# Kernel tuning notes

Hardware: AMD Instinct MI355X
Metric: run time of the kernel (lower is better)

Reference implementation:

```python
import jax, jax.numpy as jnp
import numpy as np

B, L, DIM = 2, 2048, 2048
H, KV, HD = 32, 8, 64
N_REP = H // KV


def setup_inputs() -> dict:
    key = jax.random.key(0)
    ks = jax.random.split(key, 6)
    std = DIM ** -0.5
    std_o = (H * HD) ** -0.5 / np.sqrt(2 * 24)
    x = jax.random.normal(ks[0], (B, L, DIM), dtype=jnp.float32)
    # freqs_cis packs (cos, sin), each [L, head_dim//2]
    pos = jnp.arange(L, dtype=jnp.float32)[:, None]
    inv = 1.0 / (10000.0 ** (jnp.arange(0, HD, 2, dtype=jnp.float32) / HD))
    ang = pos * inv[None, :]
    freqs_cis = jnp.stack([jnp.cos(ang), jnp.sin(ang)], axis=0)
    wq = jax.random.normal(ks[1], (H * HD, DIM), dtype=jnp.float32) * std
    wk = jax.random.normal(ks[2], (KV * HD, DIM), dtype=jnp.float32) * std
    wv = jax.random.normal(ks[3], (KV * HD, DIM), dtype=jnp.float32) * std
    wo = jax.random.normal(ks[4], (DIM, H * HD), dtype=jnp.float32) * std_o
    return {"x": x, "freqs_cis": freqs_cis, "wq": wq, "wk": wk, "wv": wv, "wo": wo}


def _rope(t, cos, sin):
    # t: [B, L, h, HD]; interleaved (real, imag) pairs in last dim
    tr = t.reshape(*t.shape[:-1], HD // 2, 2)
    out_r = tr[..., 0] * cos - tr[..., 1] * sin
    out_i = tr[..., 0] * sin + tr[..., 1] * cos
    return jnp.stack([out_r, out_i], axis=-1).reshape(t.shape)


def reference(x, freqs_cis, wq, wk, wv, wo):
    Bb, Ll, _ = x.shape
    xq = (x @ wq.T).reshape(Bb, Ll, H, HD)
    xk = (x @ wk.T).reshape(Bb, Ll, KV, HD)
    xv = (x @ wv.T).reshape(Bb, Ll, KV, HD)
    cos = freqs_cis[0].reshape(1, Ll, 1, HD // 2)
    sin = freqs_cis[1].reshape(1, Ll, 1, HD // 2)
    xq = _rope(xq, cos, sin)
    xk = _rope(xk, cos, sin)
    # GQA: repeat_interleave kv heads to n_heads
    xk = jnp.repeat(xk, N_REP, axis=2)
    xv = jnp.repeat(xv, N_REP, axis=2)
    scale = 1.0 / jnp.sqrt(jnp.asarray(HD, x.dtype))
    scores = jnp.einsum('bihd,bjhd->bhij', xq, xk) * scale
    causal = jnp.tril(jnp.ones((Ll, Ll), dtype=bool))
    scores = jnp.where(causal[None, None], scores, jnp.finfo(scores.dtype).min)
    attn = jax.nn.softmax(scores, axis=-1)
    out = jnp.einsum('bhij,bjhd->bihd', attn, xv).reshape(Bb, Ll, H * HD)
    return out @ wo.T
```

## Files before the change

kernel.cpp:

```cpp
#include <hip/hip_runtime.h>
#include <stdint.h>

typedef __bf16 bf16;
typedef __attribute__((ext_vector_type(8))) __bf16 bf16x8;
typedef __attribute__((ext_vector_type(4))) __bf16 bf16x4;
typedef __attribute__((ext_vector_type(8))) short short8v;
typedef __attribute__((ext_vector_type(4))) short short4v;
typedef __attribute__((ext_vector_type(4))) float f32x4;

static constexpr int Bn = 2, Ln = 2048, DIMn = 2048, Hn = 32, KVn = 8, HDn = 64;
static constexpr int TS = 3072;

#if defined(__has_builtin)
#if __has_builtin(__builtin_amdgcn_exp2f)
#define EXP2(x) __builtin_amdgcn_exp2f(x)
#endif
#endif
#ifndef EXP2
#define EXP2(x) exp2f(x)
#endif

#define TO_LDS(p) ((__attribute__((address_space(3))) uint32_t*)(uintptr_t)(p))
#define TO_GLB(p) ((const __attribute__((address_space(1))) uint32_t*)(uintptr_t)(p))

__global__ void cast_all(const float* __restrict__ x, const float* __restrict__ wq,
                         const float* __restrict__ wk, const float* __restrict__ wv,
                         const float* __restrict__ wo, bf16* __restrict__ xb,
                         bf16* __restrict__ wqkvb, bf16* __restrict__ wob) {
    size_t i = (size_t)(blockIdx.x * blockDim.x + threadIdx.x) * 4;
    const float* src;
    bf16* dst;
    if (i < 8388608) {
        src = x + i; dst = xb + i;
    } else if (i < 8388608 + 6291456) {
        size_t j = i - 8388608;
        dst = wqkvb + j;
        if (j < 4194304)      src = wq + j;
        else if (j < 5242880) src = wk + (j - 4194304);
        else                  src = wv + (j - 5242880);
    } else {
        size_t j = i - 14680064;
        src = wo + j; dst = wob + j;
    }
    float4 v = *(const float4*)src;
    bf16 o[4] = {(bf16)v.x, (bf16)v.y, (bf16)v.z, (bf16)v.w};
    *(uint64_t*)dst = *(uint64_t*)o;
}

__global__ void rope_k(bf16* __restrict__ qkv, const float* __restrict__ fc) {
    int idx = blockIdx.x * blockDim.x + threadIdx.x;
    int i   = idx & 31;
    int kvh = (idx >> 5) & 7;
    int bl  = idx >> 8;
    int l   = bl & (Ln - 1);
    size_t base = (size_t)bl * TS + 2048 + kvh * 64 + 2 * i;
    float cr = fc[l * 32 + i];
    float sr = fc[65536 + l * 32 + i];
    float x0 = (float)qkv[base], x1 = (float)qkv[base + 1];
    qkv[base]     = (bf16)(x0 * cr - x1 * sr);
    qkv[base + 1] = (bf16)(x0 * sr + x1 * cr);
}

static __device__ __forceinline__ void barrier_f() {
    asm volatile("" ::: "memory");
    __builtin_amdgcn_s_barrier();
    asm volatile("" ::: "memory");
}

template <int N>
static __device__ __forceinline__ void waitcnt_vm() {
    if constexpr (N == 0) asm volatile("s_waitcnt vmcnt(0)" ::: "memory");
    else if constexpr (N == 6) asm volatile("s_waitcnt vmcnt(6)" ::: "memory");
    else if constexpr (N == 7) asm volatile("s_waitcnt vmcnt(7)" ::: "memory");
    else static_assert(N == 0 || N == 6 || N == 7, "add vmcnt literal");
}

template <int BM, int BN, bool OUT_BF16>
__global__ __launch_bounds__(512, 2) void gemm256(const bf16* __restrict__ A,
                                                  const bf16* __restrict__ Bm,
                                                  void* __restrict__ C,
                                                  int M, int N, int K) {
    (void)M;
    constexpr int MI = BM / 32;
    constexpr int NI = BN / 64;
    constexpr int AJ = BM / 64, BJ = BN / 64, LPT = AJ + BJ;
    __shared__ bf16 sA[2][BM * 64];
    __shared__ bf16 sB[2][BN * 64];
    const int t    = threadIdx.x;
    const int wave = t >> 6, lane = t & 63;
    const int q4 = lane >> 4, l16 = lane & 15;
    const int wm = wave >> 2, wn = wave & 3;
    const int r8l = lane >> 3;
    const int csw = ((lane & 7) ^ r8l) * 8;

    const size_t bm = (size_t)blockIdx.y * BM, bn = (size_t)blockIdx.x * BN;
    const bf16* pa = A  + (bm + (size_t)(wave * 8 + r8l)) * K + csw;
    const bf16* pb = Bm + (bn + (size_t)(wave * 8 + r8l)) * K + csw;
    const int NT = K >> 6;

#define STGA(buf, kt)                                                                          \
    _Pragma("unroll") for (int j = 0; j < AJ; ++j)                                             \
        __builtin_amdgcn_global_load_lds(TO_GLB(pa + (size_t)j * 64 * K + (size_t)(kt) * 64),  \
                                         TO_LDS(&sA[buf][(j * 64 + wave * 8) * 64]), 16, 0, 0)
#define STGB(buf, kt)                                                                          \
    _Pragma("unroll") for (int j = 0; j < BJ; ++j)                                             \
        __builtin_amdgcn_global_load_lds(TO_GLB(pb + (size_t)j * 64 * K + (size_t)(kt) * 64),  \
                                         TO_LDS(&sB[buf][(j * 64 + wave * 8) * 64]), 16, 0, 0)

    STGA(0, 0); STGB(0, 0);
    STGA(1, 1); STGB(1, 1);
    waitcnt_vm<LPT>();
    __builtin_amdgcn_s_barrier();
    asm volatile("" ::: "memory");

    f32x4 acc[MI][NI] = {};
    bf16x8 af[MI][2], bfr[NI][2];

    for (int k = 0; k < NT; ++k) {
        const int c = k & 1;
        const bf16* la = &sA[c][0];
        const bf16* lb = &sB[c][0];
        const int sw = (l16 & 7);

#pragma unroll
        for (int mi = 0; mi < MI / 2; ++mi)
#pragma unroll
            for (int kk = 0; kk < 2; ++kk)
                af[mi][kk] = *(const bf16x8*)(la + (wm * (BM / 2) + mi * 16 + l16) * 64 +
                                              ((kk * 4 + q4) ^ sw) * 8);
#pragma unroll
        for (int ni = 0; ni < NI; ++ni)
#pragma unroll
            for (int kk = 0; kk < 2; ++kk)
                bfr[ni][kk] = *(const bf16x8*)(lb + (wn * (BN / 4) + ni * 16 + l16) * 64 +
                                               ((kk * 4 + q4) ^ sw) * 8);
#pragma unroll
        for (int mi = MI / 2; mi < MI; ++mi)
#pragma unroll
            for (int kk = 0; kk < 2; ++kk)
                af[mi][kk] = *(const bf16x8*)(la + (wm * (BM / 2) + mi * 16 + l16) * 64 +
                                              ((kk * 4 + q4) ^ sw) * 8);

        __builtin_amdgcn_s_setprio(1);
#pragma unroll
        for (int mi = 0; mi < MI; ++mi)
#pragma unroll
            for (int ni = 0; ni < NI; ++ni)
#pragma unroll
                for (int kk = 0; kk < 2; ++kk)
                    acc[mi][ni] = __builtin_amdgcn_mfma_f32_16x16x32_bf16(
                        af[mi][kk], bfr[ni][kk], acc[mi][ni], 0, 0, 0);
        __builtin_amdgcn_s_setprio(0);

        barrier_f();

        if (k + 2 < NT) {
            STGA(c, k + 2);
            STGB(c, k + 2);
            waitcnt_vm<LPT>();
        } else if (k == NT - 2) {
            waitcnt_vm<0>();
        }
        barrier_f();
    }
#undef STGA
#undef STGB

#pragma unroll
    for (int mi = 0; mi < MI; ++mi)
#pragma unroll
        for (int ni = 0; ni < NI; ++ni)
#pragma unroll
            for (int r = 0; r < 4; ++r) {
                size_t row = bm + wm * (BM / 2) + mi * 16 + q4 * 4 + r;
                size_t col = bn + wn * (BN / 4) + ni * 16 + l16;
                if (OUT_BF16)
                    ((bf16*)C)[row * (size_t)N + col] = (bf16)acc[mi][ni][r];
                else
                    ((float*)C)[row * (size_t)N + col] = acc[mi][ni][r];
            }
}

__device__ __forceinline__ int swz(int row, int colbyte) {
    return row * 128 + (colbyte ^ ((row & 7) << 4));
}

__global__ __launch_bounds__(256, 2) void attn_kernel(const bf16* __restrict__ QKV,
                                                      const float* __restrict__ fc,
                                                      bf16* __restrict__ O) {
    __shared__ bf16 sK[64 * 64];
    __shared__ bf16 sV[64 * 64];
    const int t    = threadIdx.x;
    const int wave = t >> 6, lane = t & 63;
    const int q4 = lane >> 4, l16 = lane & 15;
    const int hidx = wave & 1, qh = wave >> 1;
    const int L = blockIdx.x;
    const int pair = L & 15, hp = (L >> 4) & 1, kvh = (L >> 5) & 7, b = L >> 8;
    const int h = kvh * 4 + hp * 2 + hidx;
    constexpr float SC = 0.125f * 1.44269504088896340736f;

    const bf16* kb = QKV + (size_t)(b * Ln) * TS + 2048 + kvh * 64;
    const bf16* vb = kb + 512;
    const int krow = t >> 3;
    const int kc8  = (t & 7) * 8;
    const int kp2  = (t & 31) * 2;
    const int vh8  = (t >> 5) * 8;

    for (int half = 0; half < 2; ++half) {
        const int qtile = half == 0 ? 31 - pair : pair;

        bf16x8 qf[2][2];
#pragma unroll
        for (int g2 = 0; g2 < 2; ++g2) {
            int ql = qtile * 64 + (qh * 2 + g2) * 16 + l16;
            const bf16* qp = QKV + (size_t)(b * Ln + ql) * TS + h * 64;
#pragma unroll
            for (int hc = 0; hc < 2; ++hc) {
                bf16x8 raw = *(const bf16x8*)(qp + hc * 32 + q4 * 8);
                float4 c4 = *(const float4*)(fc + ql * 32 + hc * 16 + q4 * 4);
                float4 s4 = *(const float4*)(fc + 65536 + ql * 32 + hc * 16 + q4 * 4);
                bf16x8 o;
#pragma unroll
                for (int m = 0; m < 4; ++m) {
                    float cr = ((const float*)&c4)[m], sr = ((const float*)&s4)[m];
                    float x0 = (float)raw[2 * m], x1 = (float)raw[2 * m + 1];
                    o[2 * m]     = (bf16)((x0 * cr - x1 * sr) * SC);
                    o[2 * m + 1] = (bf16)((x0 * sr + x1 * cr) * SC);
                }
                qf[g2][hc] = o;
            }
        }

        f32x4 o_acc[2][4] = {};
        float l_r[2] = {0.f, 0.f};

        bf16x8 kreg[2], vrA, vrB;
#pragma unroll
        for (int p = 0; p < 2; ++p)
            kreg[p] = *(const bf16x8*)(kb + (size_t)(p * 32 + krow) * TS + kc8);
        vrA = *(const bf16x8*)(vb + (size_t)kp2 * TS + vh8);
        vrB = *(const bf16x8*)(vb + (size_t)(kp2 + 1) * TS + vh8);

        for (int kt = 0; kt <= qtile; ++kt) {
#pragma unroll
            for (int p = 0; p < 2; ++p) {
                int row = p * 32 + krow;
                *(float4*)((char*)sK + swz(row, kc8 * 2)) = *(float4*)&kreg[p];
            }
            {
                short8v sa = __builtin_bit_cast(short8v, vrA);
                short8v sb = __builtin_bit_cast(short8v, vrB);
#pragma unroll
                for (int j = 0; j < 8; ++j) {
                    uint32_t d = (uint32_t)(uint16_t)sa[j] |
                                 ((uint32_t)(uint16_t)sb[j] << 16);
                    *(uint32_t*)((char*)sV + swz(vh8 + j, kp2 * 2)) = d;
                }
            }
            __syncthreads();

            if (kt < qtile) {
#pragma unroll
                for (int p = 0; p < 2; ++p)
                    kreg[p] = *(const bf16x8*)(kb + (size_t)((kt + 1) * 64 + p * 32 + krow) * TS + kc8);
                vrA = *(const bf16x8*)(vb + (size_t)((kt + 1) * 64 + kp2) * TS + vh8);
                vrB = *(const bf16x8*)(vb + (size_t)((kt + 1) * 64 + kp2 + 1) * TS + vh8);
            }

            bf16x8 kf[4][2];
#pragma unroll
            for (int c = 0; c < 4; ++c)
#pragma unroll
                for (int hc = 0; hc < 2; ++hc)
                    kf[c][hc] = *(const bf16x8*)((const char*)sK +
                                                 swz(c * 16 + l16, hc * 64 + q4 * 16));
            short4v vf[4][4];
#pragma unroll
            for (int nc = 0; nc < 4; ++nc)
#pragma unroll
                for (int c = 0; c < 4; ++c)
                    vf[nc][c] = *(const short4v*)((const char*)sV +
                                                  swz(nc * 16 + l16, c * 32 + q4 * 8));

            const bool diag = (kt == qtile);
#pragma unroll
            for (int g2 = 0; g2 < 2; ++g2) {
                f32x4 s[4];
                __builtin_amdgcn_s_setprio(1);
#pragma unroll
                for (int c = 0; c < 4; ++c) {
                    f32x4 a = {};
                    a = __builtin_amdgcn_mfma_f32_16x16x32_bf16(kf[c][0], qf[g2][0], a, 0, 0, 0);
                    a = __builtin_amdgcn_mfma_f32_16x16x32_bf16(kf[c][1], qf[g2][1], a, 0, 0, 0);
                    s[c] = a;
                }
                __builtin_amdgcn_s_setprio(0);
                int qrow = qtile * 64 + (qh * 2 + g2) * 16 + l16;
                float lsum = 0.f;
                short4v pb4[4];
                if (diag) {
#pragma unroll
                    for (int c = 0; c < 4; ++c) {
                        float pc[4];
#pragma unroll
                        for (int r = 0; r < 4; ++r) {
                            float p = EXP2(s[c][r] - 12.f);
                            if (kt * 64 + c * 16 + q4 * 4 + r > qrow) p = 0.f;
                            pc[r] = p;
                            bf16 ph = (bf16)p;
                            pb4[c][r] = *(const short*)&ph;
                        }
                        lsum += (pc[0] + pc[1]) + (pc[2] + pc[3]);
                    }
                } else {
#pragma unroll
                    for (int c = 0; c < 4; ++c) {
                        float pc[4];
#pragma unroll
                        for (int r = 0; r < 4; ++r) {
                            float p = EXP2(s[c][r] - 12.f);
                            pc[r] = p;
                            bf16 ph = (bf16)p;
                            pb4[c][r] = *(const short*)&ph;
                        }
                        lsum += (pc[0] + pc[1]) + (pc[2] + pc[3]);
                    }
                }
                l_r[g2] += lsum;
                __builtin_amdgcn_s_setprio(1);
#pragma unroll
                for (int nc = 0; nc < 4; ++nc)
#pragma unroll
                    for (int c = 0; c < 4; ++c)
                        o_acc[g2][nc] = __builtin_amdgcn_mfma_f32_16x16x16bf16_1k(
                            vf[nc][c], pb4[c], o_acc[g2][nc], 0, 0, 0);
                __builtin_amdgcn_s_setprio(0);
            }
            __syncthreads();
        }

#pragma unroll
        for (int g2 = 0; g2 < 2; ++g2) {
            float l = l_r[g2];
            l += __shfl_xor(l, 16, 64);
            l += __shfl_xor(l, 32, 64);
            float inv = 1.f / l;
            int qrow = qtile * 64 + (qh * 2 + g2) * 16 + l16;
            bf16* op = O + (size_t)(b * Ln + qrow) * (Hn * HDn) + h * 64;
#pragma unroll
            for (int nc = 0; nc < 4; ++nc) {
                bf16x4 o;
#pragma unroll
                for (int r = 0; r < 4; ++r) o[r] = (bf16)(o_acc[g2][nc][r] * inv);
                *(bf16x4*)(op + nc * 16 + q4 * 4) = o;
            }
        }
    }
}

extern "C" void kernel_launch(void* const* d_in, const int* in_sizes, int n_in,
                              void* d_out, int out_size, void* d_ws, size_t ws_size,
                              hipStream_t stream) {
    const float* x  = (const float*)d_in[0];
    const float* fc = (const float*)d_in[1];
    const float* wq = (const float*)d_in[2];
    const float* wk = (const float*)d_in[3];
    const float* wv = (const float*)d_in[4];
    const float* wo = (const float*)d_in[5];
    float* out = (float*)d_out;

    const size_t T = (size_t)Bn * Ln;
    char* p = (char*)d_ws;
    bf16* xb    = (bf16*)p; p += T * DIMn * 2;
    bf16* wqkvb = (bf16*)p; p += (size_t)TS * DIMn * 2;
    bf16* wob   = (bf16*)p; p += (size_t)DIMn * Hn * HDn * 2;
    bf16* qkv   = (bf16*)p; p += T * TS * 2;
    bf16* ao    = (bf16*)p; p += T * Hn * HDn * 2;

    cast_all<<<dim3(18432), dim3(256), 0, stream>>>(x, wq, wk, wv, wo, xb, wqkvb, wob);

    gemm256<256, 192, true><<<dim3(TS / 192, 4096 / 256), dim3(512), 0, stream>>>(
        xb, wqkvb, qkv, 4096, TS, 2048);

    rope_k<<<dim3(4096), dim3(256), 0, stream>>>(qkv, fc);

    attn_kernel<<<dim3(512), dim3(256), 0, stream>>>(qkv, fc, ao);

    gemm256<128, 256, false><<<dim3(2048 / 256, 4096 / 128), dim3(512), 0, stream>>>(
        ao, wob, out, 4096, 2048, 2048);
}
```

Before: 273.1 us.

## Replace large-tile GEMM with 128x128 tile, BK=32 kernel for both projections

Replaces the templated 512-thread GEMM (256x192 / 128x256 tiles, K-step 64) with a fixed 256-thread 128x128 tile kernel using K-step 32, a new LDS swizzle, and launch bounds allowing three blocks per CU. Both the QKV projection and output projection now launch more, smaller blocks, which improves wave count and occupancy on the 256-CU device. In exchange, each block reuses less data per tile and the loop runs twice as many barrier-separated iterations with less MFMA work per sync.

New measurement: 288.8 us. 5.7% more time.

```diff
diff --git a/kernel.cpp b/kernel.cpp
--- a/kernel.cpp
+++ b/kernel.cpp
@@ -70,110 +70,93 @@
 template <int N>
 static __device__ __forceinline__ void waitcnt_vm() {
     if constexpr (N == 0) asm volatile("s_waitcnt vmcnt(0)" ::: "memory");
-    else if constexpr (N == 6) asm volatile("s_waitcnt vmcnt(6)" ::: "memory");
-    else if constexpr (N == 7) asm volatile("s_waitcnt vmcnt(7)" ::: "memory");
-    else static_assert(N == 0 || N == 6 || N == 7, "add vmcnt literal");
-}
-
-template <int BM, int BN, bool OUT_BF16>
-__global__ __launch_bounds__(512, 2) void gemm256(const bf16* __restrict__ A,
+    else if constexpr (N == 4) asm volatile("s_waitcnt vmcnt(4)" ::: "memory");
+    else static_assert(N == 0 || N == 4, "add vmcnt literal");
+}
+
+template <bool OUT_BF16>
+__global__ __launch_bounds__(256, 3) void gemm128(const bf16* __restrict__ A,
                                                   const bf16* __restrict__ Bm,
                                                   void* __restrict__ C,
                                                   int M, int N, int K) {
     (void)M;
-    constexpr int MI = BM / 32;
-    constexpr int NI = BN / 64;
-    constexpr int AJ = BM / 64, BJ = BN / 64, LPT = AJ + BJ;
-    __shared__ bf16 sA[2][BM * 64];
-    __shared__ bf16 sB[2][BN * 64];
+    __shared__ bf16 sA[2][128 * 32];
+    __shared__ bf16 sB[2][128 * 32];
     const int t    = threadIdx.x;
     const int wave = t >> 6, lane = t & 63;
     const int q4 = lane >> 4, l16 = lane & 15;
-    const int wm = wave >> 2, wn = wave & 3;
-    const int r8l = lane >> 3;
-    const int csw = ((lane & 7) ^ r8l) * 8;
-
-    const size_t bm = (size_t)blockIdx.y * BM, bn = (size_t)blockIdx.x * BN;
-    const bf16* pa = A  + (bm + (size_t)(wave * 8 + r8l)) * K + csw;
-    const bf16* pb = Bm + (bn + (size_t)(wave * 8 + r8l)) * K + csw;
-    const int NT = K >> 6;
-
-#define STGA(buf, kt)                                                                          \
-    _Pragma("unroll") for (int j = 0; j < AJ; ++j)                                             \
-        __builtin_amdgcn_global_load_lds(TO_GLB(pa + (size_t)j * 64 * K + (size_t)(kt) * 64),  \
-                                         TO_LDS(&sA[buf][(j * 64 + wave * 8) * 64]), 16, 0, 0)
-#define STGB(buf, kt)                                                                          \
-    _Pragma("unroll") for (int j = 0; j < BJ; ++j)                                             \
-        __builtin_amdgcn_global_load_lds(TO_GLB(pb + (size_t)j * 64 * K + (size_t)(kt) * 64),  \
-                                         TO_LDS(&sB[buf][(j * 64 + wave * 8) * 64]), 16, 0, 0)
-
-    STGA(0, 0); STGB(0, 0);
-    STGA(1, 1); STGB(1, 1);
-    waitcnt_vm<LPT>();
+    const int wm = wave >> 1, wn = wave & 1;
+    const int srow = lane >> 2;
+    const int scol = ((lane & 3) ^ (srow & 3)) * 8;
+
+    const size_t bm = (size_t)blockIdx.y * 128, bn = (size_t)blockIdx.x * 128;
+    const bf16* pa = A  + (bm + (size_t)(wave * 16 + srow)) * K + scol;
+    const bf16* pb = Bm + (bn + (size_t)(wave * 16 + srow)) * K + scol;
+    const int NT = K >> 5;
+
+#define STG(buf, kt)                                                                           \
+    do {                                                                                       \
+        _Pragma("unroll") for (int j = 0; j < 2; ++j) {                                        \
+            __builtin_amdgcn_global_load_lds(                                                  \
+                TO_GLB(pa + (size_t)j * 64 * K + (size_t)(kt) * 32),                           \
+                TO_LDS(&sA[buf][(j * 64 + wave * 16) * 32]), 16, 0, 0);                        \
+            __builtin_amdgcn_global_load_lds(                                                  \
+                TO_GLB(pb + (size_t)j * 64 * K + (size_t)(kt) * 32),                           \
+                TO_LDS(&sB[buf][(j * 64 + wave * 16) * 32]), 16, 0, 0);                        \
+        }                                                                                      \
+    } while (0)
+
+    STG(0, 0);
+    STG(1, 1);
+    waitcnt_vm<4>();
     __builtin_amdgcn_s_barrier();
     asm volatile("" ::: "memory");
 
-    f32x4 acc[MI][NI] = {};
-    bf16x8 af[MI][2], bfr[NI][2];
+    f32x4 acc[4][4] = {};
+    bf16x8 af[4], bfr[4];
 
     for (int k = 0; k < NT; ++k) {
         const int c = k & 1;
-        const bf16* la = &sA[c][0];
-        const bf16* lb = &sB[c][0];
-        const int sw = (l16 & 7);
-
-#pragma unroll
-        for (int mi = 0; mi < MI / 2; ++mi)
-#pragma unroll
-            for (int kk = 0; kk < 2; ++kk)
-                af[mi][kk] = *(const bf16x8*)(la + (wm * (BM / 2) + mi * 16 + l16) * 64 +
-                                              ((kk * 4 + q4) ^ sw) * 8);
-#pragma unroll
-        for (int ni = 0; ni < NI; ++ni)
-#pragma unroll
-            for (int kk = 0; kk < 2; ++kk)
-                bfr[ni][kk] = *(const bf16x8*)(lb + (wn * (BN / 4) + ni * 16 + l16) * 64 +
-                                               ((kk * 4 + q4) ^ sw) * 8);
-#pragma unroll
-        for (int mi = MI / 2; mi < MI; ++mi)
-#pragma unroll
-            for (int kk = 0; kk < 2; ++kk)
-                af[mi][kk] = *(const bf16x8*)(la + (wm * (BM / 2) + mi * 16 + l16) * 64 +
-                                              ((kk * 4 + q4) ^ sw) * 8);
+        const int sw = l16 & 3;
+
+#pragma unroll
+        for (int mi = 0; mi < 4; ++mi)
+            af[mi] = *(const bf16x8*)(&sA[c][(wm * 64 + mi * 16 + l16) * 32 +
+                                             ((q4 ^ sw) * 8)]);
+#pragma unroll
+        for (int ni = 0; ni < 4; ++ni)
+            bfr[ni] = *(const bf16x8*)(&sB[c][(wn * 64 + ni * 16 + l16) * 32 +
+                                              ((q4 ^ sw) * 8)]);
 
         __builtin_amdgcn_s_setprio(1);
 #pragma unroll
-        for (int mi = 0; mi < MI; ++mi)
-#pragma unroll
-            for (int ni = 0; ni < NI; ++ni)
-#pragma unroll
-                for (int kk = 0; kk < 2; ++kk)
-                    acc[mi][ni] = __builtin_amdgcn_mfma_f32_16x16x32_bf16(
-                        af[mi][kk], bfr[ni][kk], acc[mi][ni], 0, 0, 0);
+        for (int mi = 0; mi < 4; ++mi)
+#pragma unroll
+            for (int ni = 0; ni < 4; ++ni)
+                acc[mi][ni] = __builtin_amdgcn_mfma_f32_16x16x32_bf16(
+                    af[mi], bfr[ni], acc[mi][ni], 0, 0, 0);
         __builtin_amdgcn_s_setprio(0);
 
         barrier_f();
 
         if (k + 2 < NT) {
-            STGA(c, k + 2);
-            STGB(c, k + 2);
-            waitcnt_vm<LPT>();
+            STG(c, k + 2);
+            waitcnt_vm<4>();
         } else if (k == NT - 2) {
             waitcnt_vm<0>();
         }
         barrier_f();
     }
-#undef STGA
-#undef STGB
-
-#pragma unroll
-    for (int mi = 0; mi < MI; ++mi)
-#pragma unroll
-        for (int ni = 0; ni < NI; ++ni)
+#undef STG
+
+#pragma unroll
+    for (int mi = 0; mi < 4; ++mi)
+#pragma unroll
+        for (int ni = 0; ni < 4; ++ni)
 #pragma unroll
             for (int r = 0; r < 4; ++r) {
-                size_t row = bm + wm * (BM / 2) + mi * 16 + q4 * 4 + r;
-                size_t col = bn + wn * (BN / 4) + ni * 16 + l16;
+                size_t row = bm + wm * 64 + mi * 16 + q4 * 4 + r;
+                size_t col = bn + wn * 64 + ni * 16 + l16;
                 if (OUT_BF16)
                     ((bf16*)C)[row * (size_t)N + col] = (bf16)acc[mi][ni][r];
                 else
@@ -379,13 +362,13 @@
 
     cast_all<<<dim3(18432), dim3(256), 0, stream>>>(x, wq, wk, wv, wo, xb, wqkvb, wob);
 
-    gemm256<256, 192, true><<<dim3(TS / 192, 4096 / 256), dim3(512), 0, stream>>>(
+    gemm128<true><<<dim3(TS / 128, 4096 / 128), dim3(256), 0, stream>>>(
         xb, wqkvb, qkv, 4096, TS, 2048);
 
     rope_k<<<dim3(4096), dim3(256), 0, stream>>>(qkv, fc);
 
     attn_kernel<<<dim3(512), dim3(256), 0, stream>>>(qkv, fc, ao);
 
-    gemm256<128, 256, false><<<dim3(2048 / 256, 4096 / 128), dim3(512), 0, stream>>>(
+    gemm128<false><<<dim3(2048 / 128, 4096 / 128), dim3(256), 0, stream>>>(
         ao, wob, out, 4096, 2048, 2048);
 }
```
